# Kernel optimization log

Hardware: AMD Instinct MI355X
Metric: run time of the kernel (lower is better)

## Reference

```python
import jax, jax.numpy as jnp
import numpy as np

B, S, D = 4, 1024, 4096
HQ, HKV = 32, 8
HD = D // HQ          # 128
SCALE = HQ // HKV     # 4 (GQA repeat factor)


def setup_inputs() -> dict:
    key = jax.random.key(0)
    ks = jax.random.split(key, 11)
    s = 0.02  # init scale for weights
    return {
        "x": jax.random.normal(ks[0], (B, S, D), jnp.float32),
        # freqs_cis stored as (real, imag) pairs: [S, HD//2, 2]
        "freqs_cis": jax.random.normal(ks[1], (S, HD // 2, 2), jnp.float32),
        "Wq": jax.random.normal(ks[2], (D, HQ * HD), jnp.float32) * s,
        "bq": jnp.zeros((HQ * HD,), jnp.float32),
        "Wk": jax.random.normal(ks[3], (D, HKV * HD), jnp.float32) * s,
        "bk": jnp.zeros((HKV * HD,), jnp.float32),
        "Wv": jax.random.normal(ks[4], (D, HKV * HD), jnp.float32) * s,
        "bv": jnp.zeros((HKV * HD,), jnp.float32),
        "Wo": jax.random.normal(ks[5], (D, D), jnp.float32) * s,
        "bo": jnp.zeros((D,), jnp.float32),
        "startpos": 0,
    }


def _apply_rotary(x, fc):
    # x: [B, S, H, HD]; fc: [S, HD//2, 2] (real, imag)
    xr = x.reshape(*x.shape[:-1], HD // 2, 2)
    a, b = xr[..., 0], xr[..., 1]
    c = fc[None, :, None, :, 0]  # [1, S, 1, HD//2]
    d = fc[None, :, None, :, 1]
    # complex multiply (a+ib)*(c+id)
    out = jnp.stack([a * c - b * d, a * d + b * c], axis=-1)
    return out.reshape(x.shape)


def reference(x, freqs_cis, Wq, bq, Wk, bk, Wv, bv, Wo, bo, startpos):
    b, s, _ = x.shape
    q = (x @ Wq + bq).reshape(b, s, HQ, HD)
    k = (x @ Wk + bk).reshape(b, s, HKV, HD)
    v = (x @ Wv + bv).reshape(b, s, HKV, HD)

    fc = freqs_cis[startpos:startpos + s]
    q = _apply_rotary(q, fc)
    k = _apply_rotary(k, fc)

    # startpos == 0 and seq == cache_seq: cache write/read is identity
    q = q.transpose(0, 2, 1, 3)                            # [b, HQ, s, HD]
    k = jnp.repeat(k.transpose(0, 2, 1, 3), SCALE, axis=1)  # GQA repeat -> [b, HQ, s, HD]
    v = jnp.repeat(v.transpose(0, 2, 1, 3), SCALE, axis=1)

    scores = jnp.einsum('bhqd,bhkd->bhqk', q, k) / jnp.sqrt(jnp.float32(HD))
    causal = jnp.tril(jnp.ones((s, s), bool))
    scores = jnp.where(causal, scores, -jnp.inf)
    attn = jax.nn.softmax(scores, axis=-1)
    o = jnp.einsum('bhqk,bhkd->bhqd', attn, v)
    o = o.transpose(0, 2, 1, 3).reshape(b, s, HQ * HD)
    return o @ Wo + bo
```

## Files before the change

kernel.cpp:

```cpp
#include <hip/hip_runtime.h>
#include <hip/hip_bf16.h>

using bf16x8   = __attribute__((ext_vector_type(8))) __bf16;
using floatx4  = __attribute__((ext_vector_type(4))) float;
using floatx16 = __attribute__((ext_vector_type(16))) float;

#define DEVINL __device__ __forceinline__

DEVINL void gload16(const void* g, void* l) {
  __builtin_amdgcn_global_load_lds(
      (__attribute__((address_space(1))) void*)g,
      (__attribute__((address_space(3))) void*)l,
      16, 0, 0);
}

constexpr int S_ = 1024, D_ = 4096, HQ_ = 32, HKV_ = 8, HD_ = 128, B_ = 4;

__global__ void conv_bf16(const float* __restrict__ in, __bf16* __restrict__ out, int n) {
  int i = (blockIdx.x * 256 + threadIdx.x) * 8;
  if (i >= n) return;
  float4 a = *(const float4*)(in + i);
  float4 b = *(const float4*)(in + i + 4);
  bf16x8 o;
  o[0] = (__bf16)a.x; o[1] = (__bf16)a.y; o[2] = (__bf16)a.z; o[3] = (__bf16)a.w;
  o[4] = (__bf16)b.x; o[5] = (__bf16)b.y; o[6] = (__bf16)b.z; o[7] = (__bf16)b.w;
  *(bf16x8*)(out + i) = o;
}

__global__ void conv_transpose(const float* __restrict__ W, __bf16* __restrict__ WT, int K, int N) {
  __shared__ float tile[64][65];
  const int n0 = blockIdx.x * 64, k0 = blockIdx.y * 64;
  const int rx = threadIdx.x & 15, ry = threadIdx.x >> 4;
#pragma unroll
  for (int i = 0; i < 64; i += 16) {
    float4 v = *(const float4*)&W[(size_t)(k0 + ry + i) * N + n0 + rx * 4];
    tile[ry + i][rx * 4 + 0] = v.x;
    tile[ry + i][rx * 4 + 1] = v.y;
    tile[ry + i][rx * 4 + 2] = v.z;
    tile[ry + i][rx * 4 + 3] = v.w;
  }
  __syncthreads();
  const int wx = threadIdx.x & 7, wy = threadIdx.x >> 3;
#pragma unroll
  for (int i = 0; i < 64; i += 32) {
    bf16x8 o;
#pragma unroll
    for (int j = 0; j < 8; j++) o[j] = (__bf16)tile[wx * 8 + j][wy + i];
    *(bf16x8*)&WT[(size_t)(n0 + wy + i) * K + k0 + wx * 8] = o;
  }
}

__global__ __launch_bounds__(512, 1)
void gemm8p_qkv(const __bf16* __restrict__ A, const __bf16* __restrict__ BT,
                const float* __restrict__ b0, const float* __restrict__ b1,
                const float* __restrict__ b2, void* __restrict__ Cout,
                int M, int N, int K)
{
  __shared__ __bf16 lds[65536];
  const int t = threadIdx.x;
  const int lane = t & 63, w = t >> 6;
  const int wm = w >> 2, wn = w & 3;
  const int g = (lane >> 4) & 3, c = lane & 15;

  const int gridX = gridDim.x;
  const int nwg = gridDim.x * gridDim.y;
  int lin = blockIdx.y * gridDim.x + blockIdx.x;
  lin = (lin & 7) * (nwg >> 3) + (lin >> 3);
  const int bx = lin % gridX, by = lin / gridX;
  const int m0 = by * 256, n0 = bx * 256;

  const floatx4 zero4 = {0.f, 0.f, 0.f, 0.f};
  floatx4 acc[2][2][4][2];
#pragma unroll
  for (int a = 0; a < 2; a++)
#pragma unroll
    for (int bq = 0; bq < 2; bq++)
#pragma unroll
      for (int i = 0; i < 4; i++)
#pragma unroll
        for (int j = 0; j < 2; j++) acc[a][bq][i][j] = zero4;

  const int t3 = t >> 3;
  const int l8 = ((t & 7) ^ (t3 & 7)) * 8;
  const int browc = (t3 & 31) + ((t3 >> 5) << 6);
  const __bf16* srcA0 = A  + (size_t)(m0 + t3) * K + l8;
  const __bf16* srcA1 = A  + (size_t)(m0 + 64 + t3) * K + l8;
  const __bf16* srcB0 = BT + (size_t)(n0 + browc) * K + l8;
  const __bf16* srcB1 = BT + (size_t)(n0 + 32 + browc) * K + l8;
  const size_t k128 = (size_t)128 * K;

  const int arow_rd = (wm * 64 + c) * 64;
  const int brow_rd = (wn * 32 + c) * 64;
  const int sel0 = ((g) ^ (c & 7)) * 8;
  const int sel1 = ((4 + g) ^ (c & 7)) * 8;

  const int NT = K >> 6;

  bf16x8 af[4][2], bf0[2][2], bf1[2][2];

#define STG(srcp, subofs, kt, pbuf)                                              \
  gload16((srcp) + (size_t)(kt) * 64,        &lds[(pbuf) + (subofs) + t * 8]);   \
  gload16((srcp) + (size_t)(kt) * 64 + k128, &lds[(pbuf) + (subofs) + 4096 + t * 8]);

#define LOADA(MQ, bb)                                                            \
  _Pragma("unroll")                                                              \
  for (int i = 0; i < 4; i++) {                                                  \
    af[i][0] = *(const bf16x8*)&lds[(bb) + (MQ)*8192 + arow_rd + i*1024 + sel0]; \
    af[i][1] = *(const bf16x8*)&lds[(bb) + (MQ)*8192 + arow_rd + i*1024 + sel1]; \
  }

#define LOADB(DST, NQ, bb)                                                       \
  _Pragma("unroll")                                                              \
  for (int j = 0; j < 2; j++) {                                                  \
    DST[j][0] = *(const bf16x8*)&lds[(bb) + 16384 + (NQ)*8192 + brow_rd + j*1024 + sel0]; \
    DST[j][1] = *(const bf16x8*)&lds[(bb) + 16384 + (NQ)*8192 + brow_rd + j*1024 + sel1]; \
  }

#define MFMAQ(MQ, NQ, BF)                                                        \
  __builtin_amdgcn_s_setprio(1);                                                 \
  _Pragma("unroll")                                                              \
  for (int i = 0; i < 4; i++)                                                    \
    _Pragma("unroll")                                                            \
    for (int j = 0; j < 2; j++) {                                                \
      acc[MQ][NQ][i][j] = __builtin_amdgcn_mfma_f32_16x16x32_bf16(af[i][0], BF[j][0], acc[MQ][NQ][i][j], 0, 0, 0); \
      acc[MQ][NQ][i][j] = __builtin_amdgcn_mfma_f32_16x16x32_bf16(af[i][1], BF[j][1], acc[MQ][NQ][i][j], 0, 0, 0); \
    }                                                                            \
  __builtin_amdgcn_s_setprio(0);

#define SBAR() __builtin_amdgcn_sched_barrier(0)
#define BARR() __builtin_amdgcn_s_barrier()
#define VMC(N) asm volatile("s_waitcnt vmcnt(" #N ")" ::: "memory");
#define LGKM0() asm volatile("s_waitcnt lgkmcnt(0)" ::: "memory");

  STG(srcA0, 0, 0, 0)
  STG(srcB0, 16384, 0, 0)
  STG(srcB1, 24576, 0, 0)
  STG(srcA1, 8192, 0, 0)
  VMC(4) BARR(); SBAR();

  for (int v = 0; v < NT - 1; ++v) {
    const int bb = (v & 1) * 32768;
    const int nb = bb ^ 32768;
    LOADA(0, bb)
    LOADB(bf0, 0, bb)
    STG(srcA0, 0, v + 1, nb)
    SBAR(); VMC(4) BARR(); LGKM0() SBAR();
    MFMAQ(0, 0, bf0)
    SBAR(); BARR(); SBAR();
    LOADB(bf1, 1, bb)
    STG(srcB0, 16384, v + 1, nb)
    SBAR(); VMC(4) BARR(); LGKM0() SBAR();
    MFMAQ(0, 1, bf1)
    SBAR(); BARR(); SBAR();
    LOADA(1, bb)
    STG(srcB1, 24576, v + 1, nb)
    SBAR(); BARR(); LGKM0() SBAR();
    MFMAQ(1, 1, bf1)
    SBAR(); BARR(); SBAR();
    STG(srcA1, 8192, v + 1, nb)
    SBAR(); VMC(4) BARR(); SBAR();
    MFMAQ(1, 0, bf0)
    SBAR(); BARR(); SBAR();
  }
  {
    const int bb = ((NT - 1) & 1) * 32768;
    LOADA(0, bb)
    LOADB(bf0, 0, bb)
    SBAR(); VMC(2) BARR(); LGKM0() SBAR();
    MFMAQ(0, 0, bf0)
    SBAR(); BARR(); SBAR();
    LOADB(bf1, 1, bb)
    SBAR(); VMC(0) BARR(); LGKM0() SBAR();
    MFMAQ(0, 1, bf1)
    SBAR(); BARR(); SBAR();
    LOADA(1, bb)
    SBAR(); BARR(); LGKM0() SBAR();
    MFMAQ(1, 1, bf1)
    MFMAQ(1, 0, bf0)
  }

#undef STG
#undef LOADA
#undef LOADB
#undef MFMAQ
#undef SBAR
#undef BARR
#undef VMC
#undef LGKM0

#pragma unroll
  for (int mq = 0; mq < 2; mq++)
#pragma unroll
    for (int nq = 0; nq < 2; nq++)
#pragma unroll
      for (int j = 0; j < 2; j++) {
        const int ncol = n0 + wn * 64 + nq * 32 + j * 16 + c;
#pragma unroll
        for (int i = 0; i < 4; i++) {
          const int mbase = m0 + wm * 128 + mq * 64 + i * 16 + g * 4;
#pragma unroll
          for (int r = 0; r < 4; r++) {
            const int m = mbase + r;
            float v = acc[mq][nq][i][j][r];
            const int bb2 = m >> 10, s = m & 1023;
            __bf16* qkv = (__bf16*)Cout;
            if (ncol < 4096) {
              v += b0[ncol];
              const int h = ncol >> 7, d = ncol & 127;
              qkv[(((size_t)bb2 * 32 + h) * 1024 + s) * 128 + d] = (__bf16)v;
            } else if (ncol < 5120) {
              const int nc = ncol - 4096;
              v += b1[nc];
              const int h = nc >> 7, d = nc & 127;
              qkv[16777216 + (((size_t)bb2 * 8 + h) * 1024 + s) * 128 + d] = (__bf16)v;
            } else {
              const int nc = ncol - 5120;
              v += b2[nc];
              const int h = nc >> 7, d = nc & 127;
              qkv[20971520 + (((size_t)bb2 * 8 + h) * 128 + d) * 1024 + s] = (__bf16)v;
            }
          }
        }
      }
}

__global__ __launch_bounds__(256, 2)
void gemm_oproj(const __bf16* __restrict__ A, const __bf16* __restrict__ BT,
                const float* __restrict__ bias, float* __restrict__ Cout,
                int M, int N, int K)
{
  __shared__ __bf16 Alds[4096];
  __shared__ __bf16 Blds[4096];
  const int t = threadIdx.x;
  const int lane = t & 63;
  const int w = t >> 6;
  const int wr = w >> 1, wc = w & 1;
  const int g = lane >> 4, c = lane & 15;

  const int nwg = gridDim.x * gridDim.y;
  int lin = blockIdx.y * gridDim.x + blockIdx.x;
  lin = (lin & 7) * (nwg >> 3) + (lin >> 3);
  const int bx = lin % gridDim.x, by = lin / gridDim.x;
  const int m0 = by * 128, n0 = bx * 128;

  const floatx4 zero4 = {0.f, 0.f, 0.f, 0.f};
  floatx4 acc[4][4];
#pragma unroll
  for (int i = 0; i < 4; i++)
#pragma unroll
    for (int j = 0; j < 4; j++) acc[i][j] = zero4;

  const int srow = t >> 2;
  const int ga = (t & 3) ^ ((t >> 3) & 3);
  const __bf16* Ar = A  + (size_t)(m0 + srow) * K + ga * 8;
  const __bf16* Br = BT + (size_t)(n0 + srow) * K + ga * 8;
  const size_t rstep = (size_t)64 * K;

  const int sl = (g ^ ((c >> 1) & 3)) * 8;
  const int aoff = (wr * 64 + c) * 32 + sl;
  const int boff = (wc * 64 + c) * 32 + sl;

  for (int kt = 0; kt < K; kt += 32) {
    gload16(Ar + kt,         &Alds[t * 8]);
    gload16(Ar + rstep + kt, &Alds[(t + 256) * 8]);
    gload16(Br + kt,         &Blds[t * 8]);
    gload16(Br + rstep + kt, &Blds[(t + 256) * 8]);
    __syncthreads();
    bf16x8 af[4], bfr[4];
#pragma unroll
    for (int i = 0; i < 4; i++)
      af[i] = *(const bf16x8*)&Alds[aoff + i * 512];
#pragma unroll
    for (int j = 0; j < 4; j++)
      bfr[j] = *(const bf16x8*)&Blds[boff + j * 512];
#pragma unroll
    for (int i = 0; i < 4; i++)
#pragma unroll
      for (int j = 0; j < 4; j++)
        acc[i][j] = __builtin_amdgcn_mfma_f32_16x16x32_bf16(af[i], bfr[j], acc[i][j], 0, 0, 0);
    __syncthreads();
  }

#pragma unroll
  for (int j = 0; j < 4; j++) {
    const int ncol = n0 + wc * 64 + j * 16 + c;
    const float bv = bias[ncol];
#pragma unroll
    for (int i = 0; i < 4; i++) {
      const int mbase = m0 + wr * 64 + i * 16 + g * 4;
#pragma unroll
      for (int r = 0; r < 4; r++) {
        const int m = mbase + r;
        Cout[(size_t)m * N + ncol] = acc[i][j][r] + bv;
      }
    }
  }
}

constexpr int NQCH = B_ * HQ_ * S_ * (HD_ / 8);
constexpr int NKCH = B_ * HKV_ * S_ * (HD_ / 8);
__global__ void rope_kernel(__bf16* __restrict__ qt, __bf16* __restrict__ kt,
                            const float* __restrict__ fc, const int* __restrict__ sp) {
  int tid = blockIdx.x * 256 + threadIdx.x;
  __bf16* p;
  int idx;
  if (tid < NQCH) { p = qt; idx = tid; }
  else { idx = tid - NQCH; if (idx >= NKCH) return; p = kt; }
  const int c8 = idx & 15;
  const int s  = (idx >> 4) & 1023;
  const int srow = sp[0] + s;
  const float* f = fc + (size_t)srow * 128 + c8 * 8;
  float4 fa = *(const float4*)(f);
  float4 fb = *(const float4*)(f + 4);
  __bf16* q = p + (size_t)idx * 8;
  bf16x8 v = *(const bf16x8*)q;
  float a0 = (float)v[0], b0 = (float)v[1], a1 = (float)v[2], b1 = (float)v[3];
  float a2 = (float)v[4], b2 = (float)v[5], a3 = (float)v[6], b3 = (float)v[7];
  bf16x8 o;
  o[0] = (__bf16)(a0 * fa.x - b0 * fa.y); o[1] = (__bf16)(a0 * fa.y + b0 * fa.x);
  o[2] = (__bf16)(a1 * fa.z - b1 * fa.w); o[3] = (__bf16)(a1 * fa.w + b1 * fa.z);
  o[4] = (__bf16)(a2 * fb.x - b2 * fb.y); o[5] = (__bf16)(a2 * fb.y + b2 * fb.x);
  o[6] = (__bf16)(a3 * fb.z - b3 * fb.w); o[7] = (__bf16)(a3 * fb.w + b3 * fb.z);
  *(bf16x8*)q = o;
}

__global__ __launch_bounds__(256, 2)
void flash_attn(const __bf16* __restrict__ qt, const __bf16* __restrict__ kt,
                const __bf16* __restrict__ vt, __bf16* __restrict__ obuf)
{
  const int lane = threadIdx.x & 63, w = threadIdx.x >> 6;
  const int rl = lane & 31, hi = lane >> 5;
  const int qb = blockIdx.x & 7;
  const int bh = blockIdx.x >> 3;
  const int b = bh >> 5, h = bh & 31, hk = h >> 2;
  const int q0w = (qb + w * 8) * 32;

  const __bf16* Qp = qt + (size_t)(b * HQ_ + h) * S_ * HD_;
  const __bf16* Kp = kt + (size_t)(b * HKV_ + hk) * S_ * HD_;
  const __bf16* Vp = vt + (size_t)(b * HKV_ + hk) * HD_ * S_;

  const __bf16* Qb = Qp + (size_t)(q0w + rl) * HD_ + hi * 8;
  bf16x8 qf[8];
#pragma unroll
  for (int d = 0; d < 8; d++) qf[d] = *(const bf16x8*)(Qb + d * 16);

  const __bf16* Kb = Kp + (size_t)rl * HD_ + hi * 8;
  const __bf16* Vb = Vp + (size_t)rl * S_ + hi * 8;

  const floatx16 zero16 = {0.f,0.f,0.f,0.f,0.f,0.f,0.f,0.f,0.f,0.f,0.f,0.f,0.f,0.f,0.f,0.f};
  floatx16 oacc[4];
#pragma unroll
  for (int dt = 0; dt < 4; dt++) oacc[dt] = zero16;

  float m_run = -__builtin_inff();
  float l_run = 0.f;
  const float ksc = 0.12751744875895f;

  bf16x8 kf[8], kn[8];
#pragma unroll
  for (int d = 0; d < 8; d++) kf[d] = *(const bf16x8*)(Kb + d * 16);

  for (int kv0 = 0; kv0 <= q0w; kv0 += 32) {
    bf16x8 vf[4][2];
#pragma unroll
    for (int dt = 0; dt < 4; dt++)
#pragma unroll
      for (int kh = 0; kh < 2; kh++)
        vf[dt][kh] = *(const bf16x8*)(Vb + (size_t)dt * 32 * S_ + kv0 + kh * 16);

    floatx16 acc = zero16;
#pragma unroll
    for (int d = 0; d < 8; d++)
      acc = __builtin_amdgcn_mfma_f32_32x32x16_bf16(kf[d], qf[d], acc, 0, 0, 0);

    const int kvn = (kv0 < q0w) ? kv0 + 32 : kv0;
#pragma unroll
    for (int d = 0; d < 8; d++)
      kn[d] = *(const bf16x8*)(Kb + (size_t)kvn * HD_ + d * 16);

    if (kv0 == q0w) {
#pragma unroll
      for (int r = 0; r < 16; r++) {
        const int krel = (r & 3) + 8 * (r >> 2) + 4 * hi;
        if (krel > rl) acc[r] = -3e29f;
      }
    }

    float mx = acc[0];
#pragma unroll
    for (int r = 1; r < 16; r++) mx = fmaxf(mx, acc[r]);
    mx = fmaxf(mx, __shfl_xor(mx, 32));
    const float m_cand = mx * ksc;

    float m_use;
    const bool defer = __all(m_cand - m_run <= 8.0f);
    if (defer) {
      m_use = m_run;
    } else {
      const float m_new = fmaxf(m_run, m_cand);
      const float alpha = exp2f(m_run - m_new);
      l_run *= alpha;
      float ar[16];
#pragma unroll
      for (int r = 0; r < 16; r++)
        ar[r] = __shfl(alpha, (r & 3) + 8 * (r >> 2) + 4 * hi);
#pragma unroll
      for (int dt = 0; dt < 4; dt++)
#pragma unroll
        for (int r = 0; r < 16; r++) oacc[dt][r] *= ar[r];
      m_run = m_new;
      m_use = m_new;
    }

    float pr[16];
#pragma unroll
    for (int r = 0; r < 16; r++) pr[r] = exp2f(fmaf(acc[r], ksc, -m_use));
    float rs = pr[0];
#pragma unroll
    for (int r = 1; r < 16; r++) rs += pr[r];
    rs += __shfl_xor(rs, 32);
    l_run += rs;

    bf16x8 pa[2];
#pragma unroll
    for (int kh = 0; kh < 2; kh++) {
      const int rb = kh * 8;
      unsigned a0, b0, a1, b1;
      asm("v_cvt_pk_bf16_f32 %0, %1, %2" : "=v"(a0) : "v"(pr[rb + 0]), "v"(pr[rb + 1]));
      asm("v_cvt_pk_bf16_f32 %0, %1, %2" : "=v"(b0) : "v"(pr[rb + 4]), "v"(pr[rb + 5]));
      asm("v_cvt_pk_bf16_f32 %0, %1, %2" : "=v"(a1) : "v"(pr[rb + 2]), "v"(pr[rb + 3]));
      asm("v_cvt_pk_bf16_f32 %0, %1, %2" : "=v"(b1) : "v"(pr[rb + 6]), "v"(pr[rb + 7]));
      asm("v_permlane32_swap_b32 %0, %1" : "+v"(a0), "+v"(b0));
      asm("v_permlane32_swap_b32 %0, %1" : "+v"(a1), "+v"(b1));
      union { unsigned u[4]; bf16x8 v; } cvt;
      cvt.u[0] = a0; cvt.u[1] = a1; cvt.u[2] = b0; cvt.u[3] = b1;
      pa[kh] = cvt.v;
    }

#pragma unroll
    for (int dt = 0; dt < 4; dt++) {
      oacc[dt] = __builtin_amdgcn_mfma_f32_32x32x16_bf16(pa[0], vf[dt][0], oacc[dt], 0, 0, 0);
      oacc[dt] = __builtin_amdgcn_mfma_f32_32x32x16_bf16(pa[1], vf[dt][1], oacc[dt], 0, 0, 0);
    }

#pragma unroll
    for (int d = 0; d < 8; d++) kf[d] = kn[d];
  }

  const float linv = 1.f / l_run;
  float lr[16];
#pragma unroll
  for (int r = 0; r < 16; r++)
    lr[r] = __shfl(linv, (r & 3) + 8 * (r >> 2) + 4 * hi);
#pragma unroll
  for (int dt = 0; dt < 4; dt++)
#pragma unroll
    for (int r = 0; r < 16; r++) {
      const int qrow = q0w + (r & 3) + 8 * (r >> 2) + 4 * hi;
      const size_t o = (size_t)(b * S_ + qrow) * D_ + h * HD_ + dt * 32 + rl;
      obuf[o] = (__bf16)(oacc[dt][r] * lr[r]);
    }
}

extern "C" void kernel_launch(void* const* d_in, const int* in_sizes, int n_in,
                              void* d_out, int out_size, void* d_ws, size_t ws_size,
                              hipStream_t stream) {
  (void)in_sizes; (void)n_in; (void)out_size;
  const float* x  = (const float*)d_in[0];
  const float* fc = (const float*)d_in[1];
  const float* Wq = (const float*)d_in[2];
  const float* bq = (const float*)d_in[3];
  const float* Wk = (const float*)d_in[4];
  const float* bk = (const float*)d_in[5];
  const float* Wv = (const float*)d_in[6];
  const float* bv = (const float*)d_in[7];
  const float* Wo = (const float*)d_in[8];
  const float* bo = (const float*)d_in[9];
  const int*   sp = (const int*)d_in[10];
  float* out = (float*)d_out;

  const size_t MB = 1024 * 1024;
  if (ws_size < 192 * MB) return;
  char* ws = (char*)d_ws;
  __bf16* xb     = (__bf16*)(ws + 0);
  __bf16* WqkvT  = (__bf16*)(ws + 32 * MB);
  __bf16* WoT    = (__bf16*)(ws + 80 * MB);
  __bf16* q_t    = (__bf16*)(ws + 112 * MB);
  __bf16* k_t    = (__bf16*)(ws + 144 * MB);
  __bf16* v_t    = (__bf16*)(ws + 152 * MB);
  __bf16* ob     = (__bf16*)(ws + 160 * MB);

  conv_bf16<<<8192, 256, 0, stream>>>(x, xb, D_ * B_ * S_);
  conv_transpose<<<dim3(64, 64), 256, 0, stream>>>(Wq, WqkvT, 4096, 4096);
  conv_transpose<<<dim3(16, 64), 256, 0, stream>>>(Wk, WqkvT + (size_t)4096 * 4096, 4096, 1024);
  conv_transpose<<<dim3(16, 64), 256, 0, stream>>>(Wv, WqkvT + (size_t)5120 * 4096, 4096, 1024);
  conv_transpose<<<dim3(64, 64), 256, 0, stream>>>(Wo, WoT, 4096, 4096);

  gemm8p_qkv<<<dim3(24, 16), 512, 0, stream>>>(xb, WqkvT, bq, bk, bv, q_t, 4096, 6144, 4096);

  rope_kernel<<<(NQCH + NKCH) / 256, 256, 0, stream>>>(q_t, k_t, fc, sp);
  flash_attn<<<1024, 256, 0, stream>>>(q_t, k_t, v_t, ob);

  gemm_oproj<<<dim3(32, 32), 256, 0, stream>>>(ob, WoT, bo, out, 4096, 4096, 4096);
}
```

Before: 647.7 us.

## Fuse RoPE into QKV GEMM epilogue and remap oproj tile swizzle

Applies rotary embedding inside the QKV GEMM epilogue. Each lane gets its pair partner with a lane shuffle (the pair sits in adjacent columns), and the result is written straight to the Q/K buffers. This removes the separate rope kernel's launch and its extra read/write pass over Q and K. RoPE is now computed from fp32 accumulators instead of bf16-rounded values. The oproj GEMM also gets a new block-to-tile mapping that groups tiles by XCD into 2D regions, to improve L2 reuse.

```diff
diff --git a/kernel.cpp b/kernel.cpp
--- a/kernel.cpp
+++ b/kernel.cpp
@@ -54,6 +54,7 @@
 void gemm8p_qkv(const __bf16* __restrict__ A, const __bf16* __restrict__ BT,
                 const float* __restrict__ b0, const float* __restrict__ b1,
                 const float* __restrict__ b2, void* __restrict__ Cout,
+                const float* __restrict__ fc, const int* __restrict__ sp,
                 int M, int N, int K)
 {
   __shared__ __bf16 lds[65536];
@@ -188,6 +189,7 @@
 #undef VMC
 #undef LGKM0
 
+  const int sp0 = sp[0];
 #pragma unroll
   for (int mq = 0; mq < 2; mq++)
 #pragma unroll
@@ -201,21 +203,27 @@
 #pragma unroll
           for (int r = 0; r < 4; r++) {
             const int m = mbase + r;
+            const int bb2 = m >> 10, s = m & 1023;
             float v = acc[mq][nq][i][j][r];
-            const int bb2 = m >> 10, s = m & 1023;
+            if (ncol < 4096)       v += b0[ncol];
+            else if (ncol < 5120)  v += b1[ncol - 4096];
+            else                   v += b2[ncol - 5120];
+            const float vp = __shfl_xor(v, 1);
             __bf16* qkv = (__bf16*)Cout;
-            if (ncol < 4096) {
-              v += b0[ncol];
-              const int h = ncol >> 7, d = ncol & 127;
-              qkv[(((size_t)bb2 * 32 + h) * 1024 + s) * 128 + d] = (__bf16)v;
-            } else if (ncol < 5120) {
-              const int nc = ncol - 4096;
-              v += b1[nc];
-              const int h = nc >> 7, d = nc & 127;
-              qkv[16777216 + (((size_t)bb2 * 8 + h) * 1024 + s) * 128 + d] = (__bf16)v;
+            if (ncol < 5120) {
+              const int d = ncol & 127;
+              const float* f = fc + (((size_t)(sp0 + s)) << 7) + (d & ~1);
+              const float cs = f[0], sn = f[1];
+              v = (d & 1) ? fmaf(vp, sn, v * cs) : fmaf(v, cs, -(vp * sn));
+              if (ncol < 4096) {
+                const int h = ncol >> 7;
+                qkv[(((size_t)bb2 * 32 + h) * 1024 + s) * 128 + d] = (__bf16)v;
+              } else {
+                const int h = (ncol - 4096) >> 7;
+                qkv[16777216 + (((size_t)bb2 * 8 + h) * 1024 + s) * 128 + d] = (__bf16)v;
+              }
             } else {
               const int nc = ncol - 5120;
-              v += b2[nc];
               const int h = nc >> 7, d = nc & 127;
               qkv[20971520 + (((size_t)bb2 * 8 + h) * 128 + d) * 1024 + s] = (__bf16)v;
             }
@@ -237,10 +245,10 @@
   const int wr = w >> 1, wc = w & 1;
   const int g = lane >> 4, c = lane & 15;
 
-  const int nwg = gridDim.x * gridDim.y;
-  int lin = blockIdx.y * gridDim.x + blockIdx.x;
-  lin = (lin & 7) * (nwg >> 3) + (lin >> 3);
-  const int bx = lin % gridDim.x, by = lin / gridDim.x;
+  const int orig = blockIdx.y * gridDim.x + blockIdx.x;
+  const int xcd = orig & 7, i6 = orig >> 3;
+  const int bx = (xcd & 1) * 16 + (i6 & 15);
+  const int by = (xcd >> 1) * 8 + (i6 >> 4);
   const int m0 = by * 128, n0 = bx * 128;
 
   const floatx4 zero4 = {0.f, 0.f, 0.f, 0.f};
@@ -295,33 +303,6 @@
       }
     }
   }
-}
-
-constexpr int NQCH = B_ * HQ_ * S_ * (HD_ / 8);
-constexpr int NKCH = B_ * HKV_ * S_ * (HD_ / 8);
-__global__ void rope_kernel(__bf16* __restrict__ qt, __bf16* __restrict__ kt,
-                            const float* __restrict__ fc, const int* __restrict__ sp) {
-  int tid = blockIdx.x * 256 + threadIdx.x;
-  __bf16* p;
-  int idx;
-  if (tid < NQCH) { p = qt; idx = tid; }
-  else { idx = tid - NQCH; if (idx >= NKCH) return; p = kt; }
-  const int c8 = idx & 15;
-  const int s  = (idx >> 4) & 1023;
-  const int srow = sp[0] + s;
-  const float* f = fc + (size_t)srow * 128 + c8 * 8;
-  float4 fa = *(const float4*)(f);
-  float4 fb = *(const float4*)(f + 4);
-  __bf16* q = p + (size_t)idx * 8;
-  bf16x8 v = *(const bf16x8*)q;
-  float a0 = (float)v[0], b0 = (float)v[1], a1 = (float)v[2], b1 = (float)v[3];
-  float a2 = (float)v[4], b2 = (float)v[5], a3 = (float)v[6], b3 = (float)v[7];
-  bf16x8 o;
-  o[0] = (__bf16)(a0 * fa.x - b0 * fa.y); o[1] = (__bf16)(a0 * fa.y + b0 * fa.x);
-  o[2] = (__bf16)(a1 * fa.z - b1 * fa.w); o[3] = (__bf16)(a1 * fa.w + b1 * fa.z);
-  o[4] = (__bf16)(a2 * fb.x - b2 * fb.y); o[5] = (__bf16)(a2 * fb.y + b2 * fb.x);
-  o[6] = (__bf16)(a3 * fb.z - b3 * fb.w); o[7] = (__bf16)(a3 * fb.w + b3 * fb.z);
-  *(bf16x8*)q = o;
 }
 
 __global__ __launch_bounds__(256, 2)
@@ -496,9 +477,8 @@
   conv_transpose<<<dim3(16, 64), 256, 0, stream>>>(Wv, WqkvT + (size_t)5120 * 4096, 4096, 1024);
   conv_transpose<<<dim3(64, 64), 256, 0, stream>>>(Wo, WoT, 4096, 4096);
 
-  gemm8p_qkv<<<dim3(24, 16), 512, 0, stream>>>(xb, WqkvT, bq, bk, bv, q_t, 4096, 6144, 4096);
-
-  rope_kernel<<<(NQCH + NKCH) / 256, 256, 0, stream>>>(q_t, k_t, fc, sp);
+  gemm8p_qkv<<<dim3(24, 16), 512, 0, stream>>>(xb, WqkvT, bq, bk, bv, q_t, fc, sp, 4096, 6144, 4096);
+
   flash_attn<<<1024, 256, 0, stream>>>(q_t, k_t, v_t, ob);
 
   gemm_oproj<<<dim3(32, 32), 256, 0, stream>>>(ob, WoT, bo, out, 4096, 4096, 4096);
```

After: 645.5 us. No clear change (-0.3%).
